# Performance work log

Measured on AMD Instinct MI355X. Metric: run time of the kernel, lower is better.

## Reference

```python
import jax, jax.numpy as jnp
import numpy as np

BS, C1, NY, NX = 8, 64, 256, 256
C2, K, P = 64, 3, 1
N = 131072  # number of active (b, y, x) indices


def setup_inputs() -> dict:
    key = jax.random.key(0)
    k1, k2, k3, k4, k5, k6 = jax.random.split(key, 6)
    x = jax.random.normal(k1, (BS, C1, NY, NX), dtype=jnp.float32)
    bi = jax.random.randint(k2, (N,), 0, BS)
    yi = jax.random.randint(k3, (N,), 0, NY)
    xi = jax.random.randint(k4, (N,), 0, NX)
    indices = jnp.stack([bi, yi, xi], axis=1).astype(jnp.int32)
    weight = jax.random.normal(k5, (C2, C1, K, K), dtype=jnp.float32) * 0.05
    bias = jax.random.normal(k6, (C2,), dtype=jnp.float32) * 0.05
    return {"x": x, "indices": indices, "weight": weight, "bias": bias}


def reference(x, indices, weight, bias):
    # x: [bs, c1, ny, nx]; indices: [N, 3] of (b, y, x); weight: [c2, c1, k, k]
    bs, c1, ny, nx = x.shape
    c2, _, k, _ = weight.shape
    p = (k - 1) // 2  # asserted k == 2p + 1 in original
    xp = jnp.pad(x, ((0, 0), (0, 0), (p, p), (p, p)))  # zero-pad like F.unfold
    bi, yi, xi = indices[:, 0], indices[:, 1], indices[:, 2]
    dy = jnp.arange(k)
    dx = jnp.arange(k)
    rows = yi[:, None, None] + dy[None, :, None]  # [N, k, 1]
    cols = xi[:, None, None] + dx[None, None, :]  # [N, 1, k]
    # gather only active patches (equiv. to unfold[bi, yi, xi] in the original)
    # advanced indices at dims 0,2,3 -> result [N, k, k, c1]
    patches = xp[bi[:, None, None], :, rows, cols]
    # F.unfold channel ordering is (c1, kh, kw) flattened
    patches = patches.transpose(0, 3, 1, 2).reshape(patches.shape[0], c1 * k * k)
    w_flat = weight.reshape(c2, c1 * k * k)
    z = patches @ w_flat.T + bias  # [N, c2]
    return z
```

## Files before the change

### kernel.cpp

```cpp
#include <hip/hip_runtime.h>
#include <hip/hip_bf16.h>
#include <stdint.h>

#define NPTS 131072

typedef __attribute__((ext_vector_type(8))) short bf16x8;
typedef __attribute__((ext_vector_type(4))) float f32x4;
typedef __attribute__((ext_vector_type(8))) unsigned short u16x8;

__device__ inline unsigned short f32_to_bf16(float f) {
    union { __hip_bfloat16 h; unsigned short u; } cv;
    cv.h = __float2bfloat16(f);
    return cv.u;
}

__global__ __launch_bounds__(256) void k_prep(const float* __restrict__ x,
                                              unsigned short* __restrict__ xt,
                                              const float* __restrict__ w,
                                              unsigned short* __restrict__ wfrag) {
    if (blockIdx.x >= 2048) {
        int tid = (blockIdx.x - 2048) * 256 + threadIdx.x;
        int ci = tid >> 6;
        int l  = tid & 63;
        int q    = ci >> 3;
        int half = (ci >> 2) & 1;
        int nn   = ci & 3;
        int c2   = nn * 16 + (l & 15);
        int cin0 = half * 32 + ((l >> 4) << 3);
        u16x8 o;
#pragma unroll
        for (int e = 0; e < 8; ++e)
            o[e] = f32_to_bf16(w[c2 * 576 + (cin0 + e) * 9 + q]);
        *(u16x8*)(wfrag + tid * 8) = o;
        if (blockIdx.x == 2048 && threadIdx.x < 8) {
            u16x8 z = {};
            *(u16x8*)(xt + (size_t)8 * 65536 * 64 + threadIdx.x * 8) = z;
        }
        return;
    }

    __shared__ float tile[64][65];
    int batch   = blockIdx.x >> 8;
    int pixbase = (blockIdx.x & 255) << 8;
    int t = threadIdx.x;
    const float* xb = x + (size_t)batch * 64 * 65536;

    int c0  = t >> 4;
    int px4 = (t & 15) << 2;
    int c8  = (t & 7) << 3;
    int pp  = t >> 3;

    for (int sub = 0; sub < 4; ++sub) {
        int pix0 = pixbase + (sub << 6);
        if (sub) __syncthreads();
#pragma unroll
        for (int i = 0; i < 4; ++i) {
            int c = c0 + i * 16;
            float4 v = *(const float4*)(xb + (size_t)c * 65536 + pix0 + px4);
            tile[c][px4 + 0] = v.x; tile[c][px4 + 1] = v.y;
            tile[c][px4 + 2] = v.z; tile[c][px4 + 3] = v.w;
        }
        __syncthreads();
#pragma unroll
        for (int h = 0; h < 2; ++h) {
            int pix = pp + h * 32;
            u16x8 o;
#pragma unroll
            for (int i = 0; i < 8; ++i) o[i] = f32_to_bf16(tile[c8 + i][pix]);
            *(u16x8*)(xt + ((size_t)(batch * 65536 + pix0 + pix) * 64 + c8)) = o;
        }
    }
}

__global__ __launch_bounds__(512, 4) void k_gather_gemm(
    const unsigned short* __restrict__ xt,
    const unsigned short* __restrict__ wfrag,
    const int* __restrict__ indices,
    const float* __restrict__ bias,
    float* __restrict__ out) {
    __shared__ unsigned short wlds[72 * 512];

    int t = threadIdx.x;
    int w = t >> 6;
    int l = t & 63;
    int lo = l & 15;
    int hi = l >> 4;

#pragma unroll
    for (int i = 0; i < 9; ++i) {
        int m = t + i * 512;
        *(u16x8*)(&wlds[m * 8]) = *(const u16x8*)(wfrag + m * 8);
    }

    int p0 = blockIdx.x * 256 + w * 32;
    int pA = p0 + lo, pB = p0 + 16 + lo;
    int bA = indices[pA * 3], yA = indices[pA * 3 + 1], xA = indices[pA * 3 + 2];
    int bB = indices[pB * 3], yB = indices[pB * 3 + 1], xB = indices[pB * 3 + 2];

    const uint32_t PADOFF = (uint32_t)8 * 65536 * 128;
    uint32_t sub = (uint32_t)(hi << 4);

    auto offq = [&](int b, int y, int x, int q) -> uint32_t {
        int yy = y + (q / 3) - 1;
        int xx = x + (q % 3) - 1;
        bool v = ((unsigned)yy < 256u) & ((unsigned)xx < 256u);
        uint32_t pix = ((uint32_t)b << 16) + ((uint32_t)(yy & 255) << 8) + (uint32_t)(xx & 255);
        return (v ? pix * 128u : PADOFF) + sub;
    };
    auto lda = [&](uint32_t o) -> bf16x8 {
        return (bf16x8)(*(const u16x8*)((const char*)xt + o));
    };

    f32x4 acc[2][4];
#pragma unroll
    for (int m = 0; m < 2; ++m)
#pragma unroll
        for (int nn = 0; nn < 4; ++nn) acc[m][nn] = (f32x4)0.0f;

    __syncthreads();

    uint32_t oA = offq(bA, yA, xA, 0), oB = offq(bB, yB, xB, 0);
    bf16x8 a00 = lda(oA), a10 = lda(oB);
    bf16x8 a01 = lda(oA + 64), a11 = lda(oB + 64);

#pragma unroll
    for (int q = 0; q < 9; ++q) {
        bf16x8 n00, n10, m01, m11;
        uint32_t nA = 0, nB = 0;
        if (q < 8) {
            nA = offq(bA, yA, xA, q + 1);
            nB = offq(bB, yB, xB, q + 1);
            n00 = lda(nA); n10 = lda(nB);
        }
        const unsigned short* base = &wlds[q * 4096];
#pragma unroll
        for (int nn = 0; nn < 4; ++nn) {
            bf16x8 b0 = *(const bf16x8*)(base + nn * 512 + l * 8);
            acc[0][nn] = __builtin_amdgcn_mfma_f32_16x16x32_bf16(a00, b0, acc[0][nn], 0, 0, 0);
            acc[1][nn] = __builtin_amdgcn_mfma_f32_16x16x32_bf16(a10, b0, acc[1][nn], 0, 0, 0);
        }
        if (q < 8) { m01 = lda(nA + 64); m11 = lda(nB + 64); }
#pragma unroll
        for (int nn = 0; nn < 4; ++nn) {
            bf16x8 b1 = *(const bf16x8*)(base + 2048 + nn * 512 + l * 8);
            acc[0][nn] = __builtin_amdgcn_mfma_f32_16x16x32_bf16(a01, b1, acc[0][nn], 0, 0, 0);
            acc[1][nn] = __builtin_amdgcn_mfma_f32_16x16x32_bf16(a11, b1, acc[1][nn], 0, 0, 0);
        }
        if (q < 8) { a00 = n00; a10 = n10; a01 = m01; a11 = m11; }
    }

    int rbase = blockIdx.x * 256 + w * 32 + (hi << 2);
#pragma unroll
    for (int nn = 0; nn < 4; ++nn) {
        float bv = bias[nn * 16 + lo];
#pragma unroll
        for (int m = 0; m < 2; ++m) {
#pragma unroll
            for (int r = 0; r < 4; ++r) {
                out[(size_t)(rbase + m * 16 + r) * 64 + nn * 16 + lo] = acc[m][nn][r] + bv;
            }
        }
    }
}

__global__ void k_naive(const float* __restrict__ x, const int* __restrict__ idx,
                        const float* __restrict__ w, const float* __restrict__ bias,
                        float* __restrict__ out) {
    int i = blockIdx.x * 256 + threadIdx.x;
    if (i >= NPTS * 64) return;
    int p = i >> 6, c2 = i & 63;
    int b = idx[p * 3], yi = idx[p * 3 + 1], xi = idx[p * 3 + 2];
    float acc = bias[c2];
    for (int c = 0; c < 64; ++c) {
        const float* xp = x + ((size_t)(b * 64 + c) << 16);
        const float* wp = w + (c2 * 64 + c) * 9;
        for (int dy = 0; dy < 3; ++dy) {
            int yy = yi + dy - 1;
            if ((unsigned)yy >= 256u) continue;
            for (int dx = 0; dx < 3; ++dx) {
                int xx = xi + dx - 1;
                if ((unsigned)xx >= 256u) continue;
                acc += xp[(yy << 8) + xx] * wp[dy * 3 + dx];
            }
        }
    }
    out[i] = acc;
}

extern "C" void kernel_launch(void* const* d_in, const int* in_sizes, int n_in,
                              void* d_out, int out_size, void* d_ws, size_t ws_size,
                              hipStream_t stream) {
    const float* x       = (const float*)d_in[0];
    const int*   indices = (const int*)d_in[1];
    const float* weight  = (const float*)d_in[2];
    const float* bias    = (const float*)d_in[3];
    float* out = (float*)d_out;

    size_t xt_bytes = (size_t)8 * 65536 * 64 * 2 + 128;
    size_t need = xt_bytes + (size_t)72 * 1024;
    if (ws_size < need) {
        k_naive<<<(NPTS * 64 + 255) / 256, 256, 0, stream>>>(x, indices, weight, bias, out);
        return;
    }
    unsigned short* xt    = (unsigned short*)d_ws;
    unsigned short* wfrag = (unsigned short*)((char*)d_ws + xt_bytes);

    k_prep<<<2048 + 18, 256, 0, stream>>>(x, xt, weight, wfrag);
    k_gather_gemm<<<NPTS / 256, 512, 0, stream>>>(xt, wfrag, indices, bias, out);
}
```

Before: 64.55 us.

## Issue all gather loads upfront with one 16-point tile per wave

Each wave now handles 16 points instead of 32, and the block count doubles. Every tap offset is computed first and all 18 A-fragment global loads are issued before the MFMA loop, replacing the one-tap-ahead software prefetch. This raises the number of gathers in flight per wave to hide random-access latency. In exchange, each block reloads the 72KB weight tile into LDS for half as many points, so LDS fill traffic doubles, and holding 18 fragments raises register pressure.

```diff
diff --git a/kernel.cpp b/kernel.cpp
--- a/kernel.cpp
+++ b/kernel.cpp
@@ -92,73 +92,57 @@
         *(u16x8*)(&wlds[m * 8]) = *(const u16x8*)(wfrag + m * 8);
     }
 
-    int p0 = blockIdx.x * 256 + w * 32;
-    int pA = p0 + lo, pB = p0 + 16 + lo;
-    int bA = indices[pA * 3], yA = indices[pA * 3 + 1], xA = indices[pA * 3 + 2];
-    int bB = indices[pB * 3], yB = indices[pB * 3 + 1], xB = indices[pB * 3 + 2];
+    int pt = blockIdx.x * 128 + w * 16 + lo;
+    int b  = indices[pt * 3 + 0];
+    int yi = indices[pt * 3 + 1];
+    int xi = indices[pt * 3 + 2];
 
     const uint32_t PADOFF = (uint32_t)8 * 65536 * 128;
     uint32_t sub = (uint32_t)(hi << 4);
 
-    auto offq = [&](int b, int y, int x, int q) -> uint32_t {
-        int yy = y + (q / 3) - 1;
-        int xx = x + (q % 3) - 1;
+    uint32_t off[9];
+#pragma unroll
+    for (int q = 0; q < 9; ++q) {
+        int yy = yi + (q / 3) - 1;
+        int xx = xi + (q % 3) - 1;
         bool v = ((unsigned)yy < 256u) & ((unsigned)xx < 256u);
         uint32_t pix = ((uint32_t)b << 16) + ((uint32_t)(yy & 255) << 8) + (uint32_t)(xx & 255);
-        return (v ? pix * 128u : PADOFF) + sub;
-    };
-    auto lda = [&](uint32_t o) -> bf16x8 {
-        return (bf16x8)(*(const u16x8*)((const char*)xt + o));
-    };
+        off[q] = (v ? pix * 128u : PADOFF) + sub;
+    }
 
-    f32x4 acc[2][4];
+    bf16x8 a[18];
 #pragma unroll
-    for (int m = 0; m < 2; ++m)
+    for (int q = 0; q < 9; ++q) {
+        a[2 * q + 0] = (bf16x8)(*(const u16x8*)((const char*)xt + off[q]));
+        a[2 * q + 1] = (bf16x8)(*(const u16x8*)((const char*)xt + off[q] + 64));
+    }
+
+    f32x4 acc[4];
 #pragma unroll
-        for (int nn = 0; nn < 4; ++nn) acc[m][nn] = (f32x4)0.0f;
+    for (int nn = 0; nn < 4; ++nn) acc[nn] = (f32x4)0.0f;
 
     __syncthreads();
 
-    uint32_t oA = offq(bA, yA, xA, 0), oB = offq(bB, yB, xB, 0);
-    bf16x8 a00 = lda(oA), a10 = lda(oB);
-    bf16x8 a01 = lda(oA + 64), a11 = lda(oB + 64);
-
 #pragma unroll
     for (int q = 0; q < 9; ++q) {
-        bf16x8 n00, n10, m01, m11;
-        uint32_t nA = 0, nB = 0;
-        if (q < 8) {
-            nA = offq(bA, yA, xA, q + 1);
-            nB = offq(bB, yB, xB, q + 1);
-            n00 = lda(nA); n10 = lda(nB);
+#pragma unroll
+        for (int h = 0; h < 2; ++h) {
+            const unsigned short* base = &wlds[q * 4096 + h * 2048];
+#pragma unroll
+            for (int nn = 0; nn < 4; ++nn) {
+                bf16x8 bf = *(const bf16x8*)(base + nn * 512 + l * 8);
+                acc[nn] = __builtin_amdgcn_mfma_f32_16x16x32_bf16(a[2 * q + h], bf, acc[nn], 0, 0, 0);
+            }
         }
-        const unsigned short* base = &wlds[q * 4096];
-#pragma unroll
-        for (int nn = 0; nn < 4; ++nn) {
-            bf16x8 b0 = *(const bf16x8*)(base + nn * 512 + l * 8);
-            acc[0][nn] = __builtin_amdgcn_mfma_f32_16x16x32_bf16(a00, b0, acc[0][nn], 0, 0, 0);
-            acc[1][nn] = __builtin_amdgcn_mfma_f32_16x16x32_bf16(a10, b0, acc[1][nn], 0, 0, 0);
-        }
-        if (q < 8) { m01 = lda(nA + 64); m11 = lda(nB + 64); }
-#pragma unroll
-        for (int nn = 0; nn < 4; ++nn) {
-            bf16x8 b1 = *(const bf16x8*)(base + 2048 + nn * 512 + l * 8);
-            acc[0][nn] = __builtin_amdgcn_mfma_f32_16x16x32_bf16(a01, b1, acc[0][nn], 0, 0, 0);
-            acc[1][nn] = __builtin_amdgcn_mfma_f32_16x16x32_bf16(a11, b1, acc[1][nn], 0, 0, 0);
-        }
-        if (q < 8) { a00 = n00; a10 = n10; a01 = m01; a11 = m11; }
     }
 
-    int rbase = blockIdx.x * 256 + w * 32 + (hi << 2);
+    int rbase = blockIdx.x * 128 + w * 16 + (hi << 2);
 #pragma unroll
     for (int nn = 0; nn < 4; ++nn) {
         float bv = bias[nn * 16 + lo];
 #pragma unroll
-        for (int m = 0; m < 2; ++m) {
-#pragma unroll
-            for (int r = 0; r < 4; ++r) {
-                out[(size_t)(rbase + m * 16 + r) * 64 + nn * 16 + lo] = acc[m][nn][r] + bv;
-            }
+        for (int r = 0; r < 4; ++r) {
+            out[(size_t)(rbase + r) * 64 + nn * 16 + lo] = acc[nn][r] + bv;
         }
     }
 }
@@ -206,5 +190,5 @@
     unsigned short* wfrag = (unsigned short*)((char*)d_ws + xt_bytes);
 
     k_prep<<<2048 + 18, 256, 0, stream>>>(x, xt, weight, wfrag);
-    k_gather_gemm<<<NPTS / 256, 512, 0, stream>>>(xt, wfrag, indices, bias, out);
+    k_gather_gemm<<<NPTS / 128, 512, 0, stream>>>(xt, wfrag, indices, bias, out);
 }
```

After: 65.60 us. Within noise of the previous version (+1.6%).
